# Kernel tuning notes

Measured on AMD Instinct MI355X. Metric: run time of the kernel, lower is better.

Reference implementation:

```python
import jax, jax.numpy as jnp
import numpy as np

N, B, E = 2048, 2, 1024      # seq_len, batch, embedding_dims
H = 1024                      # hidden_dims
NH, D = 16, 64                # num_heads, head_dim (NH*D == H)
SCALE = 1.0 / float(np.sqrt(H))  # NOTE: module divides by sqrt(hidden_dims), not sqrt(head_dim)


def setup_inputs() -> dict:
    key = jax.random.key(0)
    k0, k1, k2 = jax.random.split(key, 3)
    x = jax.random.normal(k0, (N, B, E), dtype=jnp.float32)
    W_proj = jax.random.normal(k1, (E, 3 * H), dtype=jnp.float32) * 0.02
    b_proj = jnp.zeros((3 * H,), dtype=jnp.float32)
    W_out = jax.random.normal(k2, (H, E), dtype=jnp.float32) * 0.02
    b_out = jnp.zeros((E,), dtype=jnp.float32)
    return {"x": x, "W_proj": W_proj, "b_proj": b_proj, "W_out": W_out, "b_out": b_out}


def reference(x, W_proj, b_proj, W_out, b_out):
    n, b, _ = x.shape
    # QKV projection: [n, b, 3H] -> 'n b (k h d) -> k b h n d'
    proj = x @ W_proj + b_proj
    qkv = proj.reshape(n, b, 3, NH, D).transpose(2, 1, 3, 0, 4)  # [3, b, h, n, d]
    q, k, v = qkv[0], qkv[1], qkv[2]
    # scaled dot-product scores [b, h, n, n]
    scores = jnp.einsum('bhid,bhjd->bhij', q, k) * SCALE
    # causal mask: -inf above the diagonal (generate_square_subsequent_mask)
    i = jnp.arange(n)
    mask = jnp.where(i[None, :] > i[:, None], -jnp.inf, 0.0).astype(scores.dtype)
    att = jax.nn.softmax(scores + mask, axis=-1)  # dropout = identity (eval)
    out = jnp.einsum('bhij,bhjd->bhid', att, v)   # [b, h, n, d]
    out = out.transpose(2, 0, 1, 3).reshape(n, b, H)  # 'b h n d -> n b (h d)'
    return out @ W_out + b_out
```

## Files before the change

### kernel.cpp

```cpp
#include <hip/hip_runtime.h>
#include <cstdint>
#include <cstddef>

typedef __bf16 bf16_t;
typedef __bf16 bf16x8 __attribute__((ext_vector_type(8)));
typedef __bf16 bf16x4 __attribute__((ext_vector_type(4)));
typedef float f32x4 __attribute__((ext_vector_type(4)));

#define N_SEQ 2048
#define BATCH 2
#define EMB   1024
#define HID   1024
#define NHEAD 16
#define HDIM  64
#define NBROW (N_SEQ * BATCH)
#define ATT_SCALE 0.03125f
#define ATT_SCALE2 (0.03125f * 1.44269504f)

#define EXP2F(x) __builtin_amdgcn_exp2f(x)

static __device__ __forceinline__ void async_copy16(const bf16_t* g, bf16_t* l) {
  __builtin_amdgcn_global_load_lds((const __attribute__((address_space(1))) void*)g,
                                   (__attribute__((address_space(3))) void*)l,
                                   16, 0, 0);
}

__global__ void convert_bf16_kernel(const float* __restrict__ in,
                                    bf16_t* __restrict__ out) {
  int i = (blockIdx.x * 256 + threadIdx.x) * 4;
  float4 v = *(const float4*)(in + i);
  bf16x4 o;
  o[0] = (bf16_t)v.x; o[1] = (bf16_t)v.y; o[2] = (bf16_t)v.z; o[3] = (bf16_t)v.w;
  *(bf16x4*)(out + i) = o;
}

__global__ void transpose_convert_kernel(const float* __restrict__ in,
                                         bf16_t* __restrict__ out,
                                         int R, int C) {
  __shared__ float tile[32][33];
  int tx = threadIdx.x & 31, ty = threadIdx.x >> 5;
  int bc = blockIdx.x * 32, br = blockIdx.y * 32;
  #pragma unroll
  for (int i = 0; i < 32; i += 8)
    tile[ty + i][tx] = in[(size_t)(br + ty + i) * C + bc + tx];
  __syncthreads();
  #pragma unroll
  for (int i = 0; i < 32; i += 8)
    out[(size_t)(bc + ty + i) * R + br + tx] = (bf16_t)tile[tx][ty + i];
}

__global__ void vt_transpose_kernel(const bf16_t* __restrict__ Pj,
                                    bf16_t* __restrict__ Vt) {
  __shared__ bf16_t tile[32][33];
  int tx = threadIdx.x & 31, ty = threadIdx.x >> 5;
  int n0 = blockIdx.x * 32, d0 = blockIdx.y * 32;
  int bh = blockIdx.z;
  int h = bh & 15, b = bh >> 4;
  const int PJP = 3 * HID;
  #pragma unroll
  for (int i = 0; i < 32; i += 8)
    tile[ty + i][tx] = Pj[(size_t)((n0 + ty + i) * BATCH + b) * PJP + 2 * HID + h * HDIM + d0 + tx];
  __syncthreads();
  #pragma unroll
  for (int i = 0; i < 32; i += 8)
    Vt[(size_t)(bh * HDIM + d0 + ty + i) * N_SEQ + n0 + tx] = tile[tx][ty + i];
}

template <int BM, int BN, bool OUT_BF16>
__global__ __launch_bounds__(256) void gemm_bt_kernel(
    const bf16_t* __restrict__ A, const bf16_t* __restrict__ Bt,
    const float* __restrict__ bias, void* __restrict__ Cout,
    int M, int Nn, int K) {
  constexpr int MT = BM / 32;
  constexpr int NT = BN / 32;
  __shared__ __align__(16) bf16_t As[BM * 64];
  __shared__ __align__(16) bf16_t Bs[BN * 64];
  int tid = threadIdx.x;
  int wave = tid >> 6, lane = tid & 63;
  int c = lane & 15, quad = lane >> 4;
  int bm = blockIdx.x * BM;
  int bn = blockIdx.y * BN;
  int wm = (wave & 1) * (BM / 2), wn = (wave >> 1) * (BN / 2);
  f32x4 acc[MT][NT] = {};

  for (int kb = 0; kb < K; kb += 64) {
    #pragma unroll
    for (int i = 0; i < BM / 32; ++i) {
      int p = i * 256 + tid;
      int row = p >> 3, ko = (p & 7) ^ (row & 7);
      async_copy16(A + (size_t)(bm + row) * K + kb + ko * 8,
                   As + (size_t)(i * 256 + wave * 64) * 8);
    }
    #pragma unroll
    for (int i = 0; i < BN / 32; ++i) {
      int p = i * 256 + tid;
      int row = p >> 3, ko = (p & 7) ^ (row & 7);
      async_copy16(Bt + (size_t)(bn + row) * K + kb + ko * 8,
                   Bs + (size_t)(i * 256 + wave * 64) * 8);
    }
    __syncthreads();
    #pragma unroll
    for (int kk = 0; kk < 2; ++kk) {
      bf16x8 af[MT], bf[NT];
      #pragma unroll
      for (int mt = 0; mt < MT; ++mt) {
        int row = wm + mt * 16 + c;
        int slot = (kk * 4 + quad) ^ (row & 7);
        af[mt] = *(const bf16x8*)(As + (size_t)(row * 8 + slot) * 8);
      }
      #pragma unroll
      for (int nt = 0; nt < NT; ++nt) {
        int row = wn + nt * 16 + c;
        int slot = (kk * 4 + quad) ^ (row & 7);
        bf[nt] = *(const bf16x8*)(Bs + (size_t)(row * 8 + slot) * 8);
      }
      #pragma unroll
      for (int mt = 0; mt < MT; ++mt)
        #pragma unroll
        for (int nt = 0; nt < NT; ++nt)
          acc[mt][nt] = __builtin_amdgcn_mfma_f32_16x16x32_bf16(
              af[mt], bf[nt], acc[mt][nt], 0, 0, 0);
    }
    __syncthreads();
  }

  #pragma unroll
  for (int nt = 0; nt < NT; ++nt) {
    int col = bn + wn + nt * 16 + c;
    float bv = bias[col];
    #pragma unroll
    for (int mt = 0; mt < MT; ++mt) {
      #pragma unroll
      for (int r = 0; r < 4; ++r) {
        int row = bm + wm + mt * 16 + quad * 4 + r;
        float v = acc[mt][nt][r] + bv;
        if (OUT_BF16)
          ((bf16_t*)Cout)[(size_t)row * Nn + col] = (bf16_t)v;
        else
          ((float*)Cout)[(size_t)row * Nn + col] = v;
      }
    }
  }
}

__global__ __launch_bounds__(512, 4) void flash_attn_kernel(
    const bf16_t* __restrict__ Pj, const bf16_t* __restrict__ Vt,
    bf16_t* __restrict__ AO) {
  __shared__ __align__(16) bf16_t Ks[2][64 * 72];
  __shared__ __align__(16) bf16_t Vs[2][64 * 72];
  __shared__ __align__(16) bf16_t Ps[8][16 * 72];
  const int PJP = 3 * HID;
  int tid = threadIdx.x, wave = tid >> 6, lane = tid & 63;
  int c = lane & 15, quad = lane >> 4;
  int bid = blockIdx.x;
  int qb = (bid < 256) ? (15 - (bid >> 5)) : ((bid - 256) >> 5);
  int bh = bid & 31;
  int h = bh & 15, b = bh >> 4;
  int i0 = qb * 128;

  int i_row = i0 + wave * 16 + c;
  const bf16_t* qg = Pj + (size_t)(i_row * BATCH + b) * PJP + h * HDIM + quad * 8;
  bf16x8 qf0 = *(const bf16x8*)(qg);
  bf16x8 qf1 = *(const bf16x8*)(qg + 32);

  f32x4 o[4] = {};
  float mrow = -1e30f, lrow = 0.f;

  int jr = tid >> 3, dcol = (tid & 7) * 8;
  const bf16_t* kg0 = Pj + (size_t)b * PJP + HID + h * HDIM + dcol;
  const bf16_t* vg0 = Vt + (size_t)(bh * HDIM + jr) * N_SEQ + dcol;

  int njt = 2 * qb + 2;
  bf16x8 kreg = *(const bf16x8*)(kg0 + (size_t)jr * BATCH * PJP);
  bf16x8 vreg = *(const bf16x8*)(vg0);

  for (int jt = 0; jt < njt; ++jt) {
    bf16_t* ks = Ks[jt & 1];
    bf16_t* vs = Vs[jt & 1];
    *(bf16x8*)(ks + jr * 72 + dcol) = kreg;
    *(bf16x8*)(vs + jr * 72 + dcol) = vreg;
    __syncthreads();
    if (jt + 1 < njt) {
      int j0n = (jt + 1) * 64;
      kreg = *(const bf16x8*)(kg0 + (size_t)(j0n + jr) * BATCH * PJP);
      vreg = *(const bf16x8*)(vg0 + j0n);
    }

    f32x4 st[4];
    #pragma unroll
    for (int mt = 0; mt < 4; ++mt) {
      const bf16_t* kr = ks + (mt * 16 + c) * 72 + quad * 8;
      bf16x8 ka0 = *(const bf16x8*)kr;
      bf16x8 ka1 = *(const bf16x8*)(kr + 32);
      f32x4 s = {};
      s = __builtin_amdgcn_mfma_f32_16x16x32_bf16(ka0, qf0, s, 0, 0, 0);
      s = __builtin_amdgcn_mfma_f32_16x16x32_bf16(ka1, qf1, s, 0, 0, 0);
      st[mt] = s * ATT_SCALE2;
    }
    if (jt >= 2 * qb) {
      int j0 = jt * 64;
      int ig = i0 + wave * 16 + c;
      #pragma unroll
      for (int mt = 0; mt < 4; ++mt)
        #pragma unroll
        for (int r = 0; r < 4; ++r)
          if (j0 + mt * 16 + quad * 4 + r > ig) st[mt][r] = -1e30f;
    }

    float mx = st[0][0];
    #pragma unroll
    for (int mt = 0; mt < 4; ++mt)
      #pragma unroll
      for (int r = 0; r < 4; ++r) mx = fmaxf(mx, st[mt][r]);
    mx = fmaxf(mx, __shfl_xor(mx, 16));
    mx = fmaxf(mx, __shfl_xor(mx, 32));
    float mnew = fmaxf(mrow, mx);
    float alpha = EXP2F(mrow - mnew);
    mrow = mnew;
    float sum = 0.f;
    #pragma unroll
    for (int mt = 0; mt < 4; ++mt)
      #pragma unroll
      for (int r = 0; r < 4; ++r) {
        st[mt][r] = EXP2F(st[mt][r] - mnew);
        sum += st[mt][r];
      }
    sum += __shfl_xor(sum, 16);
    sum += __shfl_xor(sum, 32);
    lrow = lrow * alpha + sum;

    float ar[4];
    #pragma unroll
    for (int r = 0; r < 4; ++r) ar[r] = __shfl(alpha, quad * 4 + r);
    #pragma unroll
    for (int nt = 0; nt < 4; ++nt)
      #pragma unroll
      for (int r = 0; r < 4; ++r) o[nt][r] *= ar[r];

    bf16_t* pw = Ps[wave];
    #pragma unroll
    for (int mt = 0; mt < 4; ++mt) {
      bf16x4 pv;
      #pragma unroll
      for (int r = 0; r < 4; ++r) pv[r] = (bf16_t)st[mt][r];
      *(bf16x4*)(pw + c * 72 + mt * 16 + quad * 4) = pv;
    }
    const bf16_t* pr = pw + c * 72 + quad * 8;
    bf16x8 pa0 = *(const bf16x8*)pr;
    bf16x8 pa1 = *(const bf16x8*)(pr + 32);

    #pragma unroll
    for (int nt = 0; nt < 4; ++nt) {
      const bf16_t* vr = vs + (nt * 16 + c) * 72 + quad * 8;
      bf16x8 vb0 = *(const bf16x8*)vr;
      bf16x8 vb1 = *(const bf16x8*)(vr + 32);
      o[nt] = __builtin_amdgcn_mfma_f32_16x16x32_bf16(pa0, vb0, o[nt], 0, 0, 0);
      o[nt] = __builtin_amdgcn_mfma_f32_16x16x32_bf16(pa1, vb1, o[nt], 0, 0, 0);
    }
  }

  float lr[4];
  #pragma unroll
  for (int r = 0; r < 4; ++r) lr[r] = __shfl(lrow, quad * 4 + r);
  #pragma unroll
  for (int nt = 0; nt < 4; ++nt)
    #pragma unroll
    for (int r = 0; r < 4; ++r) {
      int i = i0 + wave * 16 + quad * 4 + r;
      AO[(size_t)(i * BATCH + b) * HID + h * HDIM + nt * 16 + c] =
          (bf16_t)(o[nt][r] / lr[r]);
    }
}

extern "C" void kernel_launch(void* const* d_in, const int* in_sizes, int n_in,
                              void* d_out, int out_size, void* d_ws, size_t ws_size,
                              hipStream_t stream) {
  const float* x      = (const float*)d_in[0];
  const float* W_proj = (const float*)d_in[1];
  const float* b_proj = (const float*)d_in[2];
  const float* W_out  = (const float*)d_in[3];
  const float* b_out  = (const float*)d_in[4];

  bf16_t* Xb  = (bf16_t*)d_ws;
  bf16_t* Wpt = Xb  + (size_t)NBROW * EMB;
  bf16_t* Wot = Wpt + (size_t)3 * HID * EMB;
  bf16_t* Pj  = Wot + (size_t)HID * EMB;
  bf16_t* AO  = Pj  + (size_t)NBROW * 3 * HID;
  bf16_t* Vt  = AO  + (size_t)NBROW * HID;

  convert_bf16_kernel<<<(NBROW * EMB) / 1024, 256, 0, stream>>>(x, Xb);
  transpose_convert_kernel<<<dim3(3 * HID / 32, EMB / 32), 256, 0, stream>>>(
      W_proj, Wpt, EMB, 3 * HID);
  transpose_convert_kernel<<<dim3(EMB / 32, HID / 32), 256, 0, stream>>>(
      W_out, Wot, HID, EMB);
  gemm_bt_kernel<128, 64, true><<<dim3(NBROW / 128, 3 * HID / 64), 256, 0, stream>>>(
      Xb, Wpt, b_proj, (void*)Pj, NBROW, 3 * HID, EMB);
  vt_transpose_kernel<<<dim3(N_SEQ / 32, HDIM / 32, BATCH * NHEAD), 256, 0, stream>>>(
      Pj, Vt);
  flash_attn_kernel<<<512, 512, 0, stream>>>(Pj, Vt, AO);
  gemm_bt_kernel<64, 64, false><<<dim3(NBROW / 64, EMB / 64), 256, 0, stream>>>(
      AO, Wot, b_out, d_out, NBROW, EMB, HID);
}
```

Before: 188.7 us.

## Swizzle flash-attention LDS, transpose PV output, and use BK=128 for out-proj GEMM

The flash-attention kernel drops padded 72-element LDS rows for K, V and P in favour of dense 64-element rows with an XOR swizzle on 16-byte octets. It also swaps the PV MFMA operand order so each lane holds output for its own query row. That removes the per-iteration alpha shuffles and the final lrow shuffles, and lets the output be written as vectorized bf16x4 stores. The GEMM gains a BK template parameter with a matching swizzle, and the output projection now uses BK=128, halving its K-loop iterations and barriers at the cost of larger LDS tiles.

```diff
diff --git a/kernel.cpp b/kernel.cpp
--- a/kernel.cpp
+++ b/kernel.cpp
@@ -14,7 +14,6 @@
 #define NHEAD 16
 #define HDIM  64
 #define NBROW (N_SEQ * BATCH)
-#define ATT_SCALE 0.03125f
 #define ATT_SCALE2 (0.03125f * 1.44269504f)
 
 #define EXP2F(x) __builtin_amdgcn_exp2f(x)
@@ -66,15 +65,17 @@
     Vt[(size_t)(bh * HDIM + d0 + ty + i) * N_SEQ + n0 + tx] = tile[tx][ty + i];
 }
 
-template <int BM, int BN, bool OUT_BF16>
+template <int BM, int BN, int BK, bool OUT_BF16>
 __global__ __launch_bounds__(256) void gemm_bt_kernel(
     const bf16_t* __restrict__ A, const bf16_t* __restrict__ Bt,
     const float* __restrict__ bias, void* __restrict__ Cout,
     int M, int Nn, int K) {
   constexpr int MT = BM / 32;
   constexpr int NT = BN / 32;
-  __shared__ __align__(16) bf16_t As[BM * 64];
-  __shared__ __align__(16) bf16_t Bs[BN * 64];
+  constexpr int OCTS = BK / 8;
+  constexpr int OM = OCTS - 1;
+  __shared__ __align__(16) bf16_t As[BM * BK];
+  __shared__ __align__(16) bf16_t Bs[BN * BK];
   int tid = threadIdx.x;
   int wave = tid >> 6, lane = tid & 63;
   int c = lane & 15, quad = lane >> 4;
@@ -83,36 +84,36 @@
   int wm = (wave & 1) * (BM / 2), wn = (wave >> 1) * (BN / 2);
   f32x4 acc[MT][NT] = {};
 
-  for (int kb = 0; kb < K; kb += 64) {
-    #pragma unroll
-    for (int i = 0; i < BM / 32; ++i) {
+  for (int kb = 0; kb < K; kb += BK) {
+    #pragma unroll
+    for (int i = 0; i < BM * OCTS / 256; ++i) {
       int p = i * 256 + tid;
-      int row = p >> 3, ko = (p & 7) ^ (row & 7);
+      int row = p >> (OCTS == 8 ? 3 : 4), ko = (p & OM) ^ (row & OM);
       async_copy16(A + (size_t)(bm + row) * K + kb + ko * 8,
                    As + (size_t)(i * 256 + wave * 64) * 8);
     }
     #pragma unroll
-    for (int i = 0; i < BN / 32; ++i) {
+    for (int i = 0; i < BN * OCTS / 256; ++i) {
       int p = i * 256 + tid;
-      int row = p >> 3, ko = (p & 7) ^ (row & 7);
+      int row = p >> (OCTS == 8 ? 3 : 4), ko = (p & OM) ^ (row & OM);
       async_copy16(Bt + (size_t)(bn + row) * K + kb + ko * 8,
                    Bs + (size_t)(i * 256 + wave * 64) * 8);
     }
     __syncthreads();
     #pragma unroll
-    for (int kk = 0; kk < 2; ++kk) {
+    for (int kk = 0; kk < BK / 32; ++kk) {
       bf16x8 af[MT], bf[NT];
       #pragma unroll
       for (int mt = 0; mt < MT; ++mt) {
         int row = wm + mt * 16 + c;
-        int slot = (kk * 4 + quad) ^ (row & 7);
-        af[mt] = *(const bf16x8*)(As + (size_t)(row * 8 + slot) * 8);
+        int slot = (kk * 4 + quad) ^ (row & OM);
+        af[mt] = *(const bf16x8*)(As + (size_t)(row * OCTS + slot) * 8);
       }
       #pragma unroll
       for (int nt = 0; nt < NT; ++nt) {
         int row = wn + nt * 16 + c;
-        int slot = (kk * 4 + quad) ^ (row & 7);
-        bf[nt] = *(const bf16x8*)(Bs + (size_t)(row * 8 + slot) * 8);
+        int slot = (kk * 4 + quad) ^ (row & OM);
+        bf[nt] = *(const bf16x8*)(Bs + (size_t)(row * OCTS + slot) * 8);
       }
       #pragma unroll
       for (int mt = 0; mt < MT; ++mt)
@@ -146,12 +147,13 @@
 __global__ __launch_bounds__(512, 4) void flash_attn_kernel(
     const bf16_t* __restrict__ Pj, const bf16_t* __restrict__ Vt,
     bf16_t* __restrict__ AO) {
-  __shared__ __align__(16) bf16_t Ks[2][64 * 72];
-  __shared__ __align__(16) bf16_t Vs[2][64 * 72];
-  __shared__ __align__(16) bf16_t Ps[8][16 * 72];
+  __shared__ __align__(16) bf16_t Ks[2][64 * 64];
+  __shared__ __align__(16) bf16_t Vs[2][64 * 64];
+  __shared__ __align__(16) bf16_t Ps[8][16 * 64];
   const int PJP = 3 * HID;
   int tid = threadIdx.x, wave = tid >> 6, lane = tid & 63;
   int c = lane & 15, quad = lane >> 4;
+  int c7 = c & 7;
   int bid = blockIdx.x;
   int qb = (bid < 256) ? (15 - (bid >> 5)) : ((bid - 256) >> 5);
   int bh = bid & 31;
@@ -166,9 +168,10 @@
   f32x4 o[4] = {};
   float mrow = -1e30f, lrow = 0.f;
 
-  int jr = tid >> 3, dcol = (tid & 7) * 8;
-  const bf16_t* kg0 = Pj + (size_t)b * PJP + HID + h * HDIM + dcol;
-  const bf16_t* vg0 = Vt + (size_t)(bh * HDIM + jr) * N_SEQ + dcol;
+  int jr = tid >> 3, oc = tid & 7;
+  int lds_off = jr * 64 + (oc ^ (jr & 7)) * 8;
+  const bf16_t* kg0 = Pj + (size_t)b * PJP + HID + h * HDIM + oc * 8;
+  const bf16_t* vg0 = Vt + (size_t)(bh * HDIM + jr) * N_SEQ + oc * 8;
 
   int njt = 2 * qb + 2;
   bf16x8 kreg = *(const bf16x8*)(kg0 + (size_t)jr * BATCH * PJP);
@@ -177,8 +180,8 @@
   for (int jt = 0; jt < njt; ++jt) {
     bf16_t* ks = Ks[jt & 1];
     bf16_t* vs = Vs[jt & 1];
-    *(bf16x8*)(ks + jr * 72 + dcol) = kreg;
-    *(bf16x8*)(vs + jr * 72 + dcol) = vreg;
+    *(bf16x8*)(ks + lds_off) = kreg;
+    *(bf16x8*)(vs + lds_off) = vreg;
     __syncthreads();
     if (jt + 1 < njt) {
       int j0n = (jt + 1) * 64;
@@ -189,9 +192,9 @@
     f32x4 st[4];
     #pragma unroll
     for (int mt = 0; mt < 4; ++mt) {
-      const bf16_t* kr = ks + (mt * 16 + c) * 72 + quad * 8;
-      bf16x8 ka0 = *(const bf16x8*)kr;
-      bf16x8 ka1 = *(const bf16x8*)(kr + 32);
+      const bf16_t* kr = ks + (mt * 16 + c) * 64;
+      bf16x8 ka0 = *(const bf16x8*)(kr + ((quad) ^ c7) * 8);
+      bf16x8 ka1 = *(const bf16x8*)(kr + ((quad + 4) ^ c7) * 8);
       f32x4 s = {};
       s = __builtin_amdgcn_mfma_f32_16x16x32_bf16(ka0, qf0, s, 0, 0, 0);
       s = __builtin_amdgcn_mfma_f32_16x16x32_bf16(ka1, qf1, s, 0, 0, 0);
@@ -229,13 +232,10 @@
     sum += __shfl_xor(sum, 32);
     lrow = lrow * alpha + sum;
 
-    float ar[4];
-    #pragma unroll
-    for (int r = 0; r < 4; ++r) ar[r] = __shfl(alpha, quad * 4 + r);
     #pragma unroll
     for (int nt = 0; nt < 4; ++nt)
       #pragma unroll
-      for (int r = 0; r < 4; ++r) o[nt][r] *= ar[r];
+      for (int r = 0; r < 4; ++r) o[nt][r] *= alpha;
 
     bf16_t* pw = Ps[wave];
     #pragma unroll
@@ -243,33 +243,32 @@
       bf16x4 pv;
       #pragma unroll
       for (int r = 0; r < 4; ++r) pv[r] = (bf16_t)st[mt][r];
-      *(bf16x4*)(pw + c * 72 + mt * 16 + quad * 4) = pv;
-    }
-    const bf16_t* pr = pw + c * 72 + quad * 8;
-    bf16x8 pa0 = *(const bf16x8*)pr;
-    bf16x8 pa1 = *(const bf16x8*)(pr + 32);
+      int joct = mt * 2 + (quad >> 1);
+      *(bf16x4*)(pw + c * 64 + (joct ^ c7) * 8 + (quad & 1) * 4) = pv;
+    }
+    const bf16_t* pr = pw + c * 64;
+    bf16x8 pa0 = *(const bf16x8*)(pr + ((quad) ^ c7) * 8);
+    bf16x8 pa1 = *(const bf16x8*)(pr + ((quad + 4) ^ c7) * 8);
 
     #pragma unroll
     for (int nt = 0; nt < 4; ++nt) {
-      const bf16_t* vr = vs + (nt * 16 + c) * 72 + quad * 8;
-      bf16x8 vb0 = *(const bf16x8*)vr;
-      bf16x8 vb1 = *(const bf16x8*)(vr + 32);
-      o[nt] = __builtin_amdgcn_mfma_f32_16x16x32_bf16(pa0, vb0, o[nt], 0, 0, 0);
-      o[nt] = __builtin_amdgcn_mfma_f32_16x16x32_bf16(pa1, vb1, o[nt], 0, 0, 0);
+      const bf16_t* vr = vs + (nt * 16 + c) * 64;
+      bf16x8 vb0 = *(const bf16x8*)(vr + ((quad) ^ c7) * 8);
+      bf16x8 vb1 = *(const bf16x8*)(vr + ((quad + 4) ^ c7) * 8);
+      o[nt] = __builtin_amdgcn_mfma_f32_16x16x32_bf16(vb0, pa0, o[nt], 0, 0, 0);
+      o[nt] = __builtin_amdgcn_mfma_f32_16x16x32_bf16(vb1, pa1, o[nt], 0, 0, 0);
     }
   }
 
-  float lr[4];
-  #pragma unroll
-  for (int r = 0; r < 4; ++r) lr[r] = __shfl(lrow, quad * 4 + r);
-  #pragma unroll
-  for (int nt = 0; nt < 4; ++nt)
-    #pragma unroll
-    for (int r = 0; r < 4; ++r) {
-      int i = i0 + wave * 16 + quad * 4 + r;
-      AO[(size_t)(i * BATCH + b) * HID + h * HDIM + nt * 16 + c] =
-          (bf16_t)(o[nt][r] / lr[r]);
-    }
+  float linv = 1.0f / lrow;
+  int orow = (size_t)0 + (i0 + wave * 16 + c) * BATCH + b;
+  #pragma unroll
+  for (int nt = 0; nt < 4; ++nt) {
+    bf16x4 pv;
+    #pragma unroll
+    for (int r = 0; r < 4; ++r) pv[r] = (bf16_t)(o[nt][r] * linv);
+    *(bf16x4*)(AO + (size_t)orow * HID + h * HDIM + nt * 16 + quad * 4) = pv;
+  }
 }
 
 extern "C" void kernel_launch(void* const* d_in, const int* in_sizes, int n_in,
@@ -293,11 +292,11 @@
       W_proj, Wpt, EMB, 3 * HID);
   transpose_convert_kernel<<<dim3(EMB / 32, HID / 32), 256, 0, stream>>>(
       W_out, Wot, HID, EMB);
-  gemm_bt_kernel<128, 64, true><<<dim3(NBROW / 128, 3 * HID / 64), 256, 0, stream>>>(
+  gemm_bt_kernel<128, 64, 64, true><<<dim3(NBROW / 128, 3 * HID / 64), 256, 0, stream>>>(
       Xb, Wpt, b_proj, (void*)Pj, NBROW, 3 * HID, EMB);
   vt_transpose_kernel<<<dim3(N_SEQ / 32, HDIM / 32, BATCH * NHEAD), 256, 0, stream>>>(
       Pj, Vt);
   flash_attn_kernel<<<512, 512, 0, stream>>>(Pj, Vt, AO);
-  gemm_bt_kernel<64, 64, false><<<dim3(NBROW / 64, EMB / 64), 256, 0, stream>>>(
+  gemm_bt_kernel<64, 64, 128, false><<<dim3(NBROW / 64, EMB / 64), 256, 0, stream>>>(
       AO, Wot, b_out, d_out, NBROW, EMB, HID);
 }
```

Result: faster. 182.5 us (-3.3%).
